# Kernel tuning notes

Measured on AMD Instinct MI355X. Metric: run time of the kernel, lower is better.

## Reference

```python
import jax, jax.numpy as jnp
import numpy as np

D_MODEL = 512
N_HEADS = 8
D_KEYS = D_MODEL // N_HEADS  # 64
DIN = D_MODEL * 2            # 1024
DPROJ = D_KEYS * N_HEADS * 2 # 1024
B, L = 2, 2048


def setup_inputs() -> dict:
    key = jax.random.key(0)
    ks = jax.random.split(key, 11)
    s_in = 1.0 / np.sqrt(DIN)
    s_out = 1.0 / np.sqrt(DPROJ)
    return {
        "queries": jax.random.normal(ks[0], (B, L, DIN), jnp.float32),
        "keys": jax.random.normal(ks[1], (B, L, DIN), jnp.float32),
        "values": jax.random.normal(ks[2], (B, L, DIN), jnp.float32),
        "Wq": jax.random.normal(ks[3], (DPROJ, DIN), jnp.float32) * s_in,
        "bq": jax.random.normal(ks[4], (DPROJ,), jnp.float32) * s_in,
        "Wk": jax.random.normal(ks[5], (DPROJ, DIN), jnp.float32) * s_in,
        "bk": jax.random.normal(ks[6], (DPROJ,), jnp.float32) * s_in,
        "Wv": jax.random.normal(ks[7], (DPROJ, DIN), jnp.float32) * s_in,
        "bv": jax.random.normal(ks[8], (DPROJ,), jnp.float32) * s_in,
        "Wo": jax.random.normal(ks[9], (DIN, DPROJ), jnp.float32) * s_out,
        "bo": jax.random.normal(ks[10], (DIN,), jnp.float32) * s_out,
    }


def reference(queries, keys, values, Wq, bq, Wk, bk, Wv, bv, Wo, bo):
    b, l, _ = queries.shape
    H, E = N_HEADS, 2
    # projections: (B, L, DIN) -> (B, L, d_keys, H, 2)
    q = (queries @ Wq.T + bq).reshape(b, l, -1, H, E)
    k = (keys @ Wk.T + bk).reshape(b, l, -1, H, E)
    v = (values @ Wv.T + bv).reshape(b, l, -1, H, E)
    scale = 1.0 / np.sqrt(E)  # E=2 (real/imag)
    # attention over the d_keys axis, per token n, per head h
    scores = jnp.einsum('bnlhe,bnshe->bnhls', q, k)  # (B, L, H, dk, dk)
    A = jax.nn.softmax(scale * scores, axis=-1)
    out = jnp.einsum('bnhls,bnshd->bnlhd', A, v)     # (B, L, dk, H, 2)
    out = out.reshape(b, l, -1)                      # (B, L, dk*H*2)
    return out @ Wo.T + bo                           # (B, L, 2*d_model)
```

## Files before the change

kernel.cpp:

```cpp
#include <hip/hip_runtime.h>
#include <hip/hip_bf16.h>
#include <stdint.h>

#define TOK   4096
#define KDIM  1024
#define NDIM  1024
#define NHEAD 8

typedef _Float16 f16;
typedef __attribute__((ext_vector_type(8))) _Float16 f16x8;
typedef __attribute__((ext_vector_type(4))) float f32x4;

__device__ __forceinline__ void gload_lds16(const void* g, void* l) {
    __builtin_amdgcn_global_load_lds(
        (const __attribute__((address_space(1))) void*)g,
        (__attribute__((address_space(3))) void*)l, 16, 0, 0);
}

struct CvtArgs {
    const float* src[7];
    f16*         dst[7];
    int          n4[7];
};

__global__ __launch_bounds__(256) void cvt_kernel(CvtArgs a) {
    const int seg = blockIdx.y;
    const float4* s = (const float4*)a.src[seg];
    f16* d = a.dst[seg];
    const int n4 = a.n4[seg];
    const int stride = gridDim.x * blockDim.x;
    for (int i = blockIdx.x * blockDim.x + threadIdx.x; i < n4; i += stride) {
        float4 v = s[i];
        union { f16 h[4]; uint2 u; } o;
        o.h[0] = (f16)v.x; o.h[1] = (f16)v.y; o.h[2] = (f16)v.z; o.h[3] = (f16)v.w;
        *(uint2*)(d + (size_t)i * 4) = o.u;
    }
}

struct GemmArgs {
    const f16*   A[3];
    const f16*   B[3];
    const float* bias[3];
    void*        C[3];
};

template<int OUTMODE>
__global__ __launch_bounds__(256) void gemm_bt_kernel(GemmArgs ga) {
    constexpr int K = KDIM, N = NDIM;
    const f16*   A    = ga.A[blockIdx.z];
    const f16*   B    = ga.B[blockIdx.z];
    const float* bias = ga.bias[blockIdx.z];

    __shared__ f16 As[128 * 64];
    __shared__ f16 Bs[64 * 64];

    const int tid  = threadIdx.x;
    const int wave = tid >> 6, lane = tid & 63;
    const int wm = wave >> 1, wn = wave & 1;
    const int bm = blockIdx.x * 128, bn = blockIdx.y * 64;
    const int lrow = lane & 15, kgrp = lane >> 4;

    f32x4 acc[4][2] = {};

    const int scol = (lane & 7) * 8;
    const int arow = wave * 32 + (lane >> 3);
    const int brow = wave * 16 + (lane >> 3);

    for (int kt = 0; kt < K; kt += 64) {
        #pragma unroll
        for (int i = 0; i < 4; ++i) {
            const int row = arow + i * 8;
            gload_lds16(A + (size_t)(bm + row) * K + kt + scol, As + row * 64 + scol);
        }
        #pragma unroll
        for (int i = 0; i < 2; ++i) {
            const int row = brow + i * 8;
            gload_lds16(B + (size_t)(bn + row) * K + kt + scol, Bs + row * 64 + scol);
        }
        __syncthreads();
        #pragma unroll
        for (int kk = 0; kk < 2; ++kk) {
            f16x8 af[4], bf[2];
            #pragma unroll
            for (int mi = 0; mi < 4; ++mi)
                af[mi] = *(const f16x8*)(As + (wm * 64 + mi * 16 + lrow) * 64 + kk * 32 + kgrp * 8);
            #pragma unroll
            for (int ni = 0; ni < 2; ++ni)
                bf[ni] = *(const f16x8*)(Bs + (wn * 32 + ni * 16 + lrow) * 64 + kk * 32 + kgrp * 8);
            #pragma unroll
            for (int mi = 0; mi < 4; ++mi)
                #pragma unroll
                for (int ni = 0; ni < 2; ++ni)
                    acc[mi][ni] = __builtin_amdgcn_mfma_f32_16x16x32_f16(af[mi], bf[ni], acc[mi][ni], 0, 0, 0);
        }
        __syncthreads();
    }

    const int rbase = kgrp * 4;
    #pragma unroll
    for (int mi = 0; mi < 4; ++mi) {
        #pragma unroll
        for (int ni = 0; ni < 2; ++ni) {
            const int col = bn + wn * 32 + ni * 16 + lrow;
            const float bv = bias[col];
            #pragma unroll
            for (int r = 0; r < 4; ++r) {
                const int row = bm + wm * 64 + mi * 16 + rbase + r;
                const float v = acc[mi][ni][r] + bv;
                if constexpr (OUTMODE == 0)
                    ((f16*)ga.C[blockIdx.z])[(size_t)row * N + col] = (f16)v;
                else
                    ((float*)ga.C[blockIdx.z])[(size_t)row * N + col] = v;
            }
        }
    }
}

__global__ __launch_bounds__(256) void attn_kernel(const f16* qp, const f16* kp,
                                                   const f16* vp, f16* ao) {
    __shared__ float2 kls[4][64];
    __shared__ float2 vls[4][64];
    const int tid = threadIdx.x, wave = tid >> 6, lane = tid & 63;
    const int task  = blockIdx.x * 4 + wave;
    const int token = task >> 3, head = task & 7;
    const size_t u = (size_t)token * 512 + head + (size_t)lane * 8;
    const float SCALE = 0.70710678118f * 1.44269504089f;

    union U2 { uint u; f16 h[2]; };
    U2 qu, ku, vu;
    qu.u = ((const uint*)qp)[u];
    ku.u = ((const uint*)kp)[u];
    vu.u = ((const uint*)vp)[u];
    const float q0 = (float)qu.h[0] * SCALE, q1 = (float)qu.h[1] * SCALE;
    kls[wave][lane] = make_float2((float)ku.h[0], (float)ku.h[1]);
    vls[wave][lane] = make_float2((float)vu.h[0], (float)vu.h[1]);
    __syncthreads();

    float sum = 0.f, o0 = 0.f, o1 = 0.f;
    #pragma unroll
    for (int s = 0; s < 64; ++s) {
        const float2 k2 = kls[wave][s];
        const float2 v2 = vls[wave][s];
        const float p = exp2f(fmaf(q0, k2.x, q1 * k2.y));
        sum += p;
        o0 = fmaf(p, v2.x, o0);
        o1 = fmaf(p, v2.y, o1);
    }
    const float inv = __builtin_amdgcn_rcpf(sum);
    U2 o;
    o.h[0] = (f16)(o0 * inv);
    o.h[1] = (f16)(o1 * inv);
    ((uint*)ao)[u] = o.u;
}

extern "C" void kernel_launch(void* const* d_in, const int* in_sizes, int n_in,
                              void* d_out, int out_size, void* d_ws, size_t ws_size,
                              hipStream_t stream) {
    const float* queries = (const float*)d_in[0];
    const float* keys    = (const float*)d_in[1];
    const float* values  = (const float*)d_in[2];
    const float* Wq = (const float*)d_in[3];
    const float* bq = (const float*)d_in[4];
    const float* Wk = (const float*)d_in[5];
    const float* bk = (const float*)d_in[6];
    const float* Wv = (const float*)d_in[7];
    const float* bv = (const float*)d_in[8];
    const float* Wo = (const float*)d_in[9];
    const float* bo = (const float*)d_in[10];

    char* ws = (char*)d_ws;
    const size_t MB = 1024 * 1024;
    f16* Xq  = (f16*)(ws + 0 * MB);
    f16* Xk  = (f16*)(ws + 8 * MB);
    f16* Xv  = (f16*)(ws + 16 * MB);
    f16* Wqh = (f16*)(ws + 24 * MB);
    f16* Wkh = (f16*)(ws + 26 * MB);
    f16* Wvh = (f16*)(ws + 28 * MB);
    f16* Woh = (f16*)(ws + 30 * MB);
    f16* qp  = (f16*)(ws + 32 * MB);
    f16* kp  = (f16*)(ws + 40 * MB);
    f16* vp  = (f16*)(ws + 48 * MB);
    f16* ao  = (f16*)(ws + 56 * MB);

    CvtArgs ca;
    ca.src[0] = queries; ca.dst[0] = Xq;  ca.n4[0] = TOK * KDIM / 4;
    ca.src[1] = keys;    ca.dst[1] = Xk;  ca.n4[1] = TOK * KDIM / 4;
    ca.src[2] = values;  ca.dst[2] = Xv;  ca.n4[2] = TOK * KDIM / 4;
    ca.src[3] = Wq;      ca.dst[3] = Wqh; ca.n4[3] = NDIM * KDIM / 4;
    ca.src[4] = Wk;      ca.dst[4] = Wkh; ca.n4[4] = NDIM * KDIM / 4;
    ca.src[5] = Wv;      ca.dst[5] = Wvh; ca.n4[5] = NDIM * KDIM / 4;
    ca.src[6] = Wo;      ca.dst[6] = Woh; ca.n4[6] = NDIM * KDIM / 4;
    cvt_kernel<<<dim3(256, 7), 256, 0, stream>>>(ca);

    GemmArgs g1;
    g1.A[0] = Xq;  g1.A[1] = Xk;  g1.A[2] = Xv;
    g1.B[0] = Wqh; g1.B[1] = Wkh; g1.B[2] = Wvh;
    g1.bias[0] = bq; g1.bias[1] = bk; g1.bias[2] = bv;
    g1.C[0] = qp; g1.C[1] = kp; g1.C[2] = vp;
    gemm_bt_kernel<0><<<dim3(32, 16, 3), 256, 0, stream>>>(g1);

    attn_kernel<<<TOK * NHEAD / 4, 256, 0, stream>>>(qp, kp, vp, ao);

    GemmArgs g2;
    g2.A[0] = ao; g2.B[0] = Woh; g2.bias[0] = bo; g2.C[0] = d_out;
    g2.A[1] = ao; g2.B[1] = Woh; g2.bias[1] = bo; g2.C[1] = d_out;
    g2.A[2] = ao; g2.B[2] = Woh; g2.bias[2] = bo; g2.C[2] = d_out;
    gemm_bt_kernel<1><<<dim3(32, 16, 1), 256, 0, stream>>>(g2);
}
```

Measured before the change: 220.7 us.

## Double-buffer GEMM LDS with XOR swizzle and coalesce attention token loads

```diff
diff --git a/kernel.cpp b/kernel.cpp
--- a/kernel.cpp
+++ b/kernel.cpp
@@ -44,15 +44,18 @@
     void*        C[3];
 };
 
+#define VM_WAIT6 asm volatile("s_waitcnt vmcnt(6)" ::: "memory")
+#define VM_WAIT0 asm volatile("s_waitcnt vmcnt(0)" ::: "memory")
+
 template<int OUTMODE>
 __global__ __launch_bounds__(256) void gemm_bt_kernel(GemmArgs ga) {
     constexpr int K = KDIM, N = NDIM;
+    constexpr int NT = K / 64;
     const f16*   A    = ga.A[blockIdx.z];
     const f16*   B    = ga.B[blockIdx.z];
     const float* bias = ga.bias[blockIdx.z];
 
-    __shared__ f16 As[128 * 64];
-    __shared__ f16 Bs[64 * 64];
+    __shared__ f16 sm[2 * (128 * 64 + 64 * 64)];
 
     const int tid  = threadIdx.x;
     const int wave = tid >> 6, lane = tid & 63;
@@ -62,38 +65,60 @@
 
     f32x4 acc[4][2] = {};
 
-    const int scol = (lane & 7) * 8;
+    const int colL = (lane & 7) << 3;
+    const int colG = (((lane & 7) ^ ((lane >> 3) & 7)) << 3);
     const int arow = wave * 32 + (lane >> 3);
     const int brow = wave * 16 + (lane >> 3);
 
-    for (int kt = 0; kt < K; kt += 64) {
+    auto stage = [&](int buf, int kt) {
+        f16* As = sm + buf * (128 * 64 + 64 * 64);
+        f16* Bs = As + 128 * 64;
         #pragma unroll
         for (int i = 0; i < 4; ++i) {
             const int row = arow + i * 8;
-            gload_lds16(A + (size_t)(bm + row) * K + kt + scol, As + row * 64 + scol);
+            gload_lds16(A + (size_t)(bm + row) * K + kt + colG, As + row * 64 + colL);
         }
         #pragma unroll
         for (int i = 0; i < 2; ++i) {
             const int row = brow + i * 8;
-            gload_lds16(B + (size_t)(bn + row) * K + kt + scol, Bs + row * 64 + scol);
-        }
-        __syncthreads();
+            gload_lds16(B + (size_t)(bn + row) * K + kt + colG, Bs + row * 64 + colL);
+        }
+    };
+
+    stage(0, 0);
+
+    const int swz = (lrow & 7) << 3;
+
+    for (int it = 0; it < NT; ++it) {
+        const int cur = it & 1;
+        if (it + 1 < NT) {
+            stage(cur ^ 1, (it + 1) * 64);
+            VM_WAIT6;
+        } else {
+            VM_WAIT0;
+        }
+        __builtin_amdgcn_s_barrier();
+        __builtin_amdgcn_sched_barrier(0);
+
+        const f16* As = sm + cur * (128 * 64 + 64 * 64);
+        const f16* Bs = As + 128 * 64;
         #pragma unroll
         for (int kk = 0; kk < 2; ++kk) {
             f16x8 af[4], bf[2];
+            const int kcol = (kk * 32 + kgrp * 8) ^ swz;
             #pragma unroll
             for (int mi = 0; mi < 4; ++mi)
-                af[mi] = *(const f16x8*)(As + (wm * 64 + mi * 16 + lrow) * 64 + kk * 32 + kgrp * 8);
+                af[mi] = *(const f16x8*)(As + (wm * 64 + mi * 16 + lrow) * 64 + kcol);
             #pragma unroll
             for (int ni = 0; ni < 2; ++ni)
-                bf[ni] = *(const f16x8*)(Bs + (wn * 32 + ni * 16 + lrow) * 64 + kk * 32 + kgrp * 8);
+                bf[ni] = *(const f16x8*)(Bs + (wn * 32 + ni * 16 + lrow) * 64 + kcol);
             #pragma unroll
             for (int mi = 0; mi < 4; ++mi)
                 #pragma unroll
                 for (int ni = 0; ni < 2; ++ni)
                     acc[mi][ni] = __builtin_amdgcn_mfma_f32_16x16x32_f16(af[mi], bf[ni], acc[mi][ni], 0, 0, 0);
         }
-        __syncthreads();
+        __builtin_amdgcn_s_barrier();
     }
 
     const int rbase = kgrp * 4;
@@ -116,41 +141,41 @@
     }
 }
 
-__global__ __launch_bounds__(256) void attn_kernel(const f16* qp, const f16* kp,
+__global__ __launch_bounds__(512) void attn_kernel(const f16* qp, const f16* kp,
                                                    const f16* vp, f16* ao) {
-    __shared__ float2 kls[4][64];
-    __shared__ float2 vls[4][64];
-    const int tid = threadIdx.x, wave = tid >> 6, lane = tid & 63;
-    const int task  = blockIdx.x * 4 + wave;
-    const int token = task >> 3, head = task & 7;
-    const size_t u = (size_t)token * 512 + head + (size_t)lane * 8;
+    __shared__ uint qls[512], kls[512], vls[512], ols[512];
+    const int tid = threadIdx.x, head = tid >> 6, lane = tid & 63;
+    const int token = blockIdx.x;
+    const size_t base = (size_t)token * 512;
     const float SCALE = 0.70710678118f * 1.44269504089f;
 
+    qls[tid] = ((const uint*)qp)[base + tid];
+    kls[tid] = ((const uint*)kp)[base + tid];
+    vls[tid] = ((const uint*)vp)[base + tid];
+    __syncthreads();
+
     union U2 { uint u; f16 h[2]; };
-    U2 qu, ku, vu;
-    qu.u = ((const uint*)qp)[u];
-    ku.u = ((const uint*)kp)[u];
-    vu.u = ((const uint*)vp)[u];
+    U2 qu; qu.u = qls[lane * 8 + head];
     const float q0 = (float)qu.h[0] * SCALE, q1 = (float)qu.h[1] * SCALE;
-    kls[wave][lane] = make_float2((float)ku.h[0], (float)ku.h[1]);
-    vls[wave][lane] = make_float2((float)vu.h[0], (float)vu.h[1]);
-    __syncthreads();
 
     float sum = 0.f, o0 = 0.f, o1 = 0.f;
     #pragma unroll
     for (int s = 0; s < 64; ++s) {
-        const float2 k2 = kls[wave][s];
-        const float2 v2 = vls[wave][s];
-        const float p = exp2f(fmaf(q0, k2.x, q1 * k2.y));
+        U2 ku, vu;
+        ku.u = kls[s * 8 + head];
+        vu.u = vls[s * 8 + head];
+        const float p = exp2f(fmaf(q0, (float)ku.h[0], q1 * (float)ku.h[1]));
         sum += p;
-        o0 = fmaf(p, v2.x, o0);
-        o1 = fmaf(p, v2.y, o1);
+        o0 = fmaf(p, (float)vu.h[0], o0);
+        o1 = fmaf(p, (float)vu.h[1], o1);
     }
     const float inv = __builtin_amdgcn_rcpf(sum);
     U2 o;
     o.h[0] = (f16)(o0 * inv);
     o.h[1] = (f16)(o1 * inv);
-    ((uint*)ao)[u] = o.u;
+    ols[lane * 8 + head] = o.u;
+    __syncthreads();
+    ((uint*)ao)[base + tid] = ols[tid];
 }
 
 extern "C" void kernel_launch(void* const* d_in, const int* in_sizes, int n_in,
@@ -199,7 +224,7 @@
     g1.C[0] = qp; g1.C[1] = kp; g1.C[2] = vp;
     gemm_bt_kernel<0><<<dim3(32, 16, 3), 256, 0, stream>>>(g1);
 
-    attn_kernel<<<TOK * NHEAD / 4, 256, 0, stream>>>(qp, kp, vp, ao);
+    attn_kernel<<<TOK, 512, 0, stream>>>(qp, kp, vp, ao);
 
     GemmArgs g2;
     g2.A[0] = ao; g2.B[0] = Woh; g2.bias[0] = bo; g2.C[0] = d_out;
```

After: 210.1 us. -4.8%, faster.
